# Optimization experiments

Measured on AMD Instinct MI355X. Metric: run time of the kernel, lower is better.

Reference implementation:

```python
import jax, jax.numpy as jnp
import numpy as np

N_POINTS = 300000
N_PAIRS = 100000  # rulebook pairs per kernel offset
K_OFFSETS = 27    # 3x3x3 kernel
C_IN, C_OUT = 32, 64
GROUPS = 8
EPS = 1e-5
NEG_SLOPE = 0.01


def setup_inputs() -> dict:
    key = jax.random.key(0)
    k1, k2, k3, k4 = jax.random.split(key, 4)
    feats = jax.random.normal(k1, (N_POINTS, C_IN), dtype=jnp.float32)
    weight = jax.random.normal(k2, (K_OFFSETS, C_IN, C_OUT), dtype=jnp.float32) * (1.0 / np.sqrt(C_IN * K_OFFSETS))
    gamma = jnp.ones((C_OUT,), dtype=jnp.float32)
    beta = jnp.zeros((C_OUT,), dtype=jnp.float32)
    in_idx = jax.random.randint(k3, (K_OFFSETS, N_PAIRS), 0, N_POINTS, dtype=jnp.int64)
    out_idx = jax.random.randint(k4, (K_OFFSETS, N_PAIRS), 0, N_POINTS, dtype=jnp.int64)
    return {"feats": feats, "weight": weight, "gamma": gamma, "beta": beta,
            "in_idx": in_idx, "out_idx": out_idx}


def reference(feats, weight, gamma, beta, in_idx, out_idx):
    # Sparse 3D conv via rulebook: gather -> per-offset matmul -> scatter-add
    gathered = feats[in_idx]                       # [K, P, C_in]
    y = jnp.einsum('kpi,kio->kpo', gathered, weight)  # [K, P, C_out]
    out = jnp.zeros((feats.shape[0], weight.shape[2]), feats.dtype)
    out = out.at[out_idx.reshape(-1)].add(y.reshape(-1, weight.shape[2]))
    # GroupNorm(8, C_out): stats over all points and channels within each group
    N, C = out.shape
    xg = out.reshape(N, GROUPS, C // GROUPS)
    mean = jnp.mean(xg, axis=(0, 2), keepdims=True)
    var = jnp.var(xg, axis=(0, 2), keepdims=True)
    xn = ((xg - mean) * jax.lax.rsqrt(var + EPS)).reshape(N, C)
    xn = xn * gamma + beta
    # LeakyReLU (default negative_slope = 0.01)
    return jnp.where(xn >= 0, xn, NEG_SLOPE * xn)
```

## Files before the change

kernel.cpp:

```cpp
#include <hip/hip_runtime.h>

#define NPTS   300000
#define NPAIRS 100000
#define KOFF   27
#define NTOT   (KOFF * NPAIRS)
#define CIN    32
#define COUT   64
#define NGROUP 8
#define EPSV   1e-5f
#define SLOPE  0.01f

#define PAIRS_PER_BLOCK 256
#define BLOCKS_PER_K ((NPAIRS + PAIRS_PER_BLOCK - 1) / PAIRS_PER_BLOCK)

#define NB1 293

#define OFS_STATS  0u
#define OFS_CURSOR 4096u
#define OFS_PART   (OFS_CURSOR + 1200128u)
#define OFS_PSLOT  (OFS_PART + 8192u)
#define OFS_SLOTS  (OFS_PSLOT + 10800128u)
#define OFS_FB16   (OFS_SLOTS + 345600000u)
#define WS_NEEDED  ((size_t)OFS_FB16 + 19200000u)

__device__ inline unsigned short f2b(float x) {
    unsigned u = __float_as_uint(x);
    u += 0x7FFFu + ((u >> 16) & 1u);
    return (unsigned short)(u >> 16);
}
__device__ inline float b2f_lo(unsigned d)  { return __uint_as_float(d << 16); }
__device__ inline float b2f_hi(unsigned d)  { return __uint_as_float(d & 0xFFFF0000u); }


__global__ __launch_bounds__(256) void to_bf16_kernel(const float2* __restrict__ src,
                                                      unsigned* __restrict__ dst, int n2) {
    int i = blockIdx.x * 256 + threadIdx.x;
    if (i < n2) {
        float2 v = src[i];
        dst[i] = (unsigned)f2b(v.x) | ((unsigned)f2b(v.y) << 16);
    }
}

__global__ __launch_bounds__(256) void zero_aux_kernel(int* __restrict__ cursor,
                                                       float* __restrict__ stats) {
    int i = blockIdx.x * 256 + threadIdx.x;
    if (i < NPTS) cursor[i] = 0;
    if (blockIdx.x == 0 && threadIdx.x < 16) stats[threadIdx.x] = 0.f;
}

__global__ __launch_bounds__(256) void hist_kernel(const int* __restrict__ oi,
                                                   int* __restrict__ cursor) {
    int i = blockIdx.x * 256 + threadIdx.x;
    if (i < NTOT) atomicAdd(cursor + oi[i], 1);
}

__global__ __launch_bounds__(256) void reduce_blocks_kernel(const int* __restrict__ cursor,
                                                            int* __restrict__ part) {
    __shared__ int sm[256];
    int tid = threadIdx.x, i0 = blockIdx.x * 1024 + tid * 4;
    int s = 0;
#pragma unroll
    for (int j = 0; j < 4; ++j) if (i0 + j < NPTS) s += cursor[i0 + j];
    sm[tid] = s; __syncthreads();
    for (int off = 128; off; off >>= 1) {
        if (tid < off) sm[tid] += sm[tid + off];
        __syncthreads();
    }
    if (tid == 0) part[blockIdx.x] = sm[0];
}

__global__ __launch_bounds__(512) void scan_partials_kernel(int* __restrict__ part) {
    __shared__ int sm[512];
    int tid = threadIdx.x;
    int v = (tid < NB1) ? part[tid] : 0;
    sm[tid] = v; __syncthreads();
    for (int off = 1; off < 512; off <<= 1) {
        int t = (tid >= off) ? sm[tid - off] : 0;
        __syncthreads();
        sm[tid] += t;
        __syncthreads();
    }
    if (tid < NB1) part[tid] = sm[tid] - v;
}

__global__ __launch_bounds__(256) void scan_apply_kernel(int* __restrict__ cursor,
                                                         const int* __restrict__ part) {
    __shared__ int sm[256];
    int tid = threadIdx.x, i0 = blockIdx.x * 1024 + tid * 4;
    int c0 = 0, c1 = 0, c2 = 0, c3 = 0;
    if (i0 + 0 < NPTS) c0 = cursor[i0 + 0];
    if (i0 + 1 < NPTS) c1 = cursor[i0 + 1];
    if (i0 + 2 < NPTS) c2 = cursor[i0 + 2];
    if (i0 + 3 < NPTS) c3 = cursor[i0 + 3];
    int s = c0 + c1 + c2 + c3;
    sm[tid] = s; __syncthreads();
    for (int off = 1; off < 256; off <<= 1) {
        int t = (tid >= off) ? sm[tid - off] : 0;
        __syncthreads();
        sm[tid] += t;
        __syncthreads();
    }
    int excl = sm[tid] - s + part[blockIdx.x];
    if (i0 + 0 < NPTS) cursor[i0 + 0] = excl;
    if (i0 + 1 < NPTS) cursor[i0 + 1] = excl + c0;
    if (i0 + 2 < NPTS) cursor[i0 + 2] = excl + c0 + c1;
    if (i0 + 3 < NPTS) cursor[i0 + 3] = excl + c0 + c1 + c2;
}

__global__ __launch_bounds__(256) void fill_kernel(const int* __restrict__ oi,
                                                   int* __restrict__ cursor,
                                                   int* __restrict__ pair_slot) {
    int i = blockIdx.x * 256 + threadIdx.x;
    if (i < NTOT) pair_slot[i] = atomicAdd(cursor + oi[i], 1);
}

__global__ __launch_bounds__(256) void convA_kernel(
    const unsigned* __restrict__ fb16, const float* __restrict__ weight,
    const int* __restrict__ in_idx, const int* __restrict__ pair_slot,
    unsigned short* __restrict__ slots16)
{
    const int lane = threadIdx.x & 63;
    const int wave = threadIdx.x >> 6;
    const int k     = blockIdx.x / BLOCKS_PER_K;
    const int pair0 = (blockIdx.x % BLOCKS_PER_K) * PAIRS_PER_BLOCK;

    float w[CIN];
    const float* wk = weight + k * (CIN * COUT) + lane;
#pragma unroll
    for (int i = 0; i < CIN; ++i) w[i] = wk[i * COUT];

    const int per_wave = PAIRS_PER_BLOCK / 4;
    int p    = pair0 + wave * per_wave;
    int pend = p + per_wave;
    if (pend > NPAIRS) pend = NPAIRS;

    const int* ii = in_idx    + k * NPAIRS;
    const int* ps = pair_slot + k * NPAIRS;

    for (; p < pend; ++p) {
        int rin  = __builtin_amdgcn_readfirstlane(ii[p]);
        int slot = __builtin_amdgcn_readfirstlane(ps[p]);
        const unsigned* fr = fb16 + rin * (CIN / 2);
        float acc = 0.f;
#pragma unroll
        for (int j = 0; j < CIN / 2; ++j) {
            unsigned d = fr[j];
            acc = fmaf(b2f_lo(d), w[2 * j],     acc);
            acc = fmaf(b2f_hi(d), w[2 * j + 1], acc);
        }
        slots16[(size_t)slot * COUT + lane] = f2b(acc);
    }
}

__global__ __launch_bounds__(256) void reduceB_kernel(const unsigned short* __restrict__ slots16,
                                                      const int* __restrict__ ends,
                                                      float* __restrict__ out)
{
    const int lane = threadIdx.x & 63;
    const int row  = blockIdx.x * 4 + (threadIdx.x >> 6);
    if (row >= NPTS) return;
    int e = ends[row];
    int s = (row == 0) ? 0 : ends[row - 1];
    float acc = 0.f;
    for (; s < e; ++s)
        acc += __uint_as_float(((unsigned)slots16[(size_t)s * COUT + lane]) << 16);
    out[(size_t)row * COUT + lane] = acc;
}

__global__ __launch_bounds__(256) void stats_kernel(const float* __restrict__ out,
                                                    float* __restrict__ stats) {
    const int c = threadIdx.x & 63;
    const int wave_in_grid = blockIdx.x * 4 + (threadIdx.x >> 6);
    const int nwaves = gridDim.x * 4;
    float s = 0.f, ss = 0.f;
    for (int r = wave_in_grid; r < NPTS; r += nwaves) {
        float v = out[(size_t)r * COUT + c];
        s += v; ss += v * v;
    }
#pragma unroll
    for (int m = 1; m < 8; m <<= 1) {
        s  += __shfl_xor(s,  m, 64);
        ss += __shfl_xor(ss, m, 64);
    }
    if ((c & 7) == 0) {
        int g = c >> 3;
        atomicAdd(stats + g,     s);
        atomicAdd(stats + 8 + g, ss);
    }
}

__global__ __launch_bounds__(256) void norm_kernel(float4* __restrict__ out4, int n4,
                                                   const float* __restrict__ stats,
                                                   const float* __restrict__ gamma,
                                                   const float* __restrict__ beta) {
    int i = blockIdx.x * blockDim.x + threadIdx.x;
    if (i >= n4) return;
    int c0 = (i & 15) * 4;
    int g  = c0 >> 3;
    const float cnt = (float)NPTS * (COUT / NGROUP);
    float mean = stats[g] / cnt;
    float var  = stats[8 + g] / cnt - mean * mean;
    float inv  = rsqrtf(var + EPSV);
    float4 v  = out4[i];
    float4 ga = *(const float4*)(gamma + c0);
    float4 be = *(const float4*)(beta  + c0);
    float x;
    x = (v.x - mean) * inv * ga.x + be.x; v.x = x >= 0.f ? x : SLOPE * x;
    x = (v.y - mean) * inv * ga.y + be.y; v.y = x >= 0.f ? x : SLOPE * x;
    x = (v.z - mean) * inv * ga.z + be.z; v.z = x >= 0.f ? x : SLOPE * x;
    x = (v.w - mean) * inv * ga.w + be.w; v.w = x >= 0.f ? x : SLOPE * x;
    out4[i] = v;
}

__global__ __launch_bounds__(256) void zero_out_kernel(float4* __restrict__ out4, int n4,
                                                       float* __restrict__ stats) {
    int i = blockIdx.x * blockDim.x + threadIdx.x;
    if (i < n4) out4[i] = make_float4(0.f, 0.f, 0.f, 0.f);
    if (blockIdx.x == 0 && threadIdx.x < 16) stats[threadIdx.x] = 0.f;
}

__global__ __launch_bounds__(256) void conv_atomic_kernel(
    const float* __restrict__ feats, const float* __restrict__ weight,
    const int* __restrict__ in_idx, const int* __restrict__ out_idx,
    float* __restrict__ out)
{
    const int lane = threadIdx.x & 63;
    const int wave = threadIdx.x >> 6;
    const int k     = blockIdx.x / BLOCKS_PER_K;
    const int pair0 = (blockIdx.x % BLOCKS_PER_K) * PAIRS_PER_BLOCK;
    float w[CIN];
    const float* wk = weight + k * (CIN * COUT) + lane;
#pragma unroll
    for (int i = 0; i < CIN; ++i) w[i] = wk[i * COUT];
    const int per_wave = PAIRS_PER_BLOCK / 4;
    int p = pair0 + wave * per_wave;
    int pend = p + per_wave;
    if (pend > NPAIRS) pend = NPAIRS;
    const int* ii = in_idx  + k * NPAIRS;
    const int* oi = out_idx + k * NPAIRS;
    for (; p < pend; ++p) {
        int rin  = __builtin_amdgcn_readfirstlane(ii[p]);
        int rout = __builtin_amdgcn_readfirstlane(oi[p]);
        const float* frow = feats + (size_t)rin * CIN;
        float acc = 0.f;
#pragma unroll
        for (int i = 0; i < CIN; ++i) acc = fmaf(frow[i], w[i], acc);
        atomicAdd(out + (size_t)rout * COUT + lane, acc);
    }
}

extern "C" void kernel_launch(void* const* d_in, const int* in_sizes, int n_in,
                              void* d_out, int out_size, void* d_ws, size_t ws_size,
                              hipStream_t stream) {
    const float* feats   = (const float*)d_in[0];
    const float* weight  = (const float*)d_in[1];
    const float* gamma   = (const float*)d_in[2];
    const float* beta    = (const float*)d_in[3];
    const int*   in_idx  = (const int*)d_in[4];
    const int*   out_idx = (const int*)d_in[5];
    float* out = (float*)d_out;

    char* ws = (char*)d_ws;
    float*          stats     = (float*)(ws + OFS_STATS);
    int*            cursor    = (int*)(ws + OFS_CURSOR);
    int*            part      = (int*)(ws + OFS_PART);
    int*            pair_slot = (int*)(ws + OFS_PSLOT);
    unsigned short* slots16   = (unsigned short*)(ws + OFS_SLOTS);
    unsigned*       fb16      = (unsigned*)(ws + OFS_FB16);

    int n4 = out_size / 4;
    int zb = (n4 + 255) / 256;

    if (ws_size >= WS_NEEDED) {
        int n2 = NPTS * CIN / 2;
        to_bf16_kernel<<<(n2 + 255) / 256, 256, 0, stream>>>((const float2*)feats, fb16, n2);
        zero_aux_kernel<<<(NPTS + 255) / 256, 256, 0, stream>>>(cursor, stats);
        hist_kernel<<<(NTOT + 255) / 256, 256, 0, stream>>>(out_idx, cursor);
        reduce_blocks_kernel<<<NB1, 256, 0, stream>>>(cursor, part);
        scan_partials_kernel<<<1, 512, 0, stream>>>(part);
        scan_apply_kernel<<<NB1, 256, 0, stream>>>(cursor, part);
        fill_kernel<<<(NTOT + 255) / 256, 256, 0, stream>>>(out_idx, cursor, pair_slot);
        convA_kernel<<<KOFF * BLOCKS_PER_K, 256, 0, stream>>>(fb16, weight, in_idx, pair_slot, slots16);
        reduceB_kernel<<<(NPTS + 3) / 4, 256, 0, stream>>>(slots16, cursor, out);
        stats_kernel<<<1024, 256, 0, stream>>>(out, stats);
        norm_kernel<<<zb, 256, 0, stream>>>((float4*)out, n4, stats, gamma, beta);
    } else {
        zero_out_kernel<<<zb, 256, 0, stream>>>((float4*)out, n4, stats);
        conv_atomic_kernel<<<KOFF * BLOCKS_PER_K, 256, 0, stream>>>(feats, weight, in_idx, out_idx, out);
        stats_kernel<<<1024, 256, 0, stream>>>(out, stats);
        norm_kernel<<<zb, 256, 0, stream>>>((float4*)out, n4, stats, gamma, beta);
    }
}
```

Baseline: 823.8 us.

## Replace slot-buffer scatter with CSR gather-conv fused with GroupNorm stats

The counting sort now stores packed (input index, offset) entries per output row instead of per-pair slot indices. A single CSR kernel walks each output row's entries, gathers fp16 features, and computes dot products against fp16 weights held in LDS using fdot2. It writes each output row once and accumulates the GroupNorm statistics in the same pass. This removes the large intermediate slots buffer and the separate reduce and stats kernels, at the cost of fp16 precision, a static per-wave row split that can load-balance poorly, and a sequential per-row loop.

Result: slower. 847.1 us (+2.8%).

```diff
diff --git a/kernel.cpp b/kernel.cpp
--- a/kernel.cpp
+++ b/kernel.cpp
@@ -12,33 +12,49 @@
 
 #define PAIRS_PER_BLOCK 256
 #define BLOCKS_PER_K ((NPAIRS + PAIRS_PER_BLOCK - 1) / PAIRS_PER_BLOCK)
-
 #define NB1 293
 
 #define OFS_STATS  0u
 #define OFS_CURSOR 4096u
-#define OFS_PART   (OFS_CURSOR + 1200128u)
-#define OFS_PSLOT  (OFS_PART + 8192u)
-#define OFS_SLOTS  (OFS_PSLOT + 10800128u)
-#define OFS_FB16   (OFS_SLOTS + 345600000u)
-#define WS_NEEDED  ((size_t)OFS_FB16 + 19200000u)
-
+#define OFS_PART   (OFS_CURSOR + 1204224u)
+#define OFS_ENT    (OFS_PART + 4096u)
+#define OFS_FH16   (OFS_ENT + 10850304u)
+#define WS_MAIN    ((size_t)OFS_FH16 + 19200000u)
+#define OFS_FB16_FB 4096u
+#define WS_BF16_FB ((size_t)OFS_FB16_FB + 19200000u)
+
+typedef _Float16 half2v __attribute__((ext_vector_type(2)));
+
+__device__ inline unsigned pack_h2(float a, float b) {
+    union { _Float16 h[2]; unsigned u; } x;
+    x.h[0] = (_Float16)a; x.h[1] = (_Float16)b;
+    return x.u;
+}
+__device__ inline half2v as_h2(unsigned u) {
+    union { unsigned u; half2v h; } x; x.u = u; return x.h;
+}
+__device__ inline float dot2_h(unsigned a, unsigned b, float c) {
+#if __has_builtin(__builtin_amdgcn_fdot2)
+    return __builtin_amdgcn_fdot2(as_h2(a), as_h2(b), c, false);
+#else
+    half2v ha = as_h2(a), hb = as_h2(b);
+    c = fmaf((float)ha.x, (float)hb.x, c);
+    return fmaf((float)ha.y, (float)hb.y, c);
+#endif
+}
 __device__ inline unsigned short f2b(float x) {
     unsigned u = __float_as_uint(x);
     u += 0x7FFFu + ((u >> 16) & 1u);
     return (unsigned short)(u >> 16);
 }
-__device__ inline float b2f_lo(unsigned d)  { return __uint_as_float(d << 16); }
-__device__ inline float b2f_hi(unsigned d)  { return __uint_as_float(d & 0xFFFF0000u); }
-
-
-__global__ __launch_bounds__(256) void to_bf16_kernel(const float2* __restrict__ src,
-                                                      unsigned* __restrict__ dst, int n2) {
-    int i = blockIdx.x * 256 + threadIdx.x;
-    if (i < n2) {
-        float2 v = src[i];
-        dst[i] = (unsigned)f2b(v.x) | ((unsigned)f2b(v.y) << 16);
-    }
+__device__ inline float b2f_lo(unsigned d) { return __uint_as_float(d << 16); }
+__device__ inline float b2f_hi(unsigned d) { return __uint_as_float(d & 0xFFFF0000u); }
+
+
+__global__ __launch_bounds__(256) void to_f16_kernel(const float2* __restrict__ src,
+                                                     unsigned* __restrict__ dst, int n2) {
+    int i = blockIdx.x * 256 + threadIdx.x;
+    if (i < n2) { float2 v = src[i]; dst[i] = pack_h2(v.x, v.y); }
 }
 
 __global__ __launch_bounds__(256) void zero_aux_kernel(int* __restrict__ cursor,
@@ -108,84 +124,84 @@
 }
 
 __global__ __launch_bounds__(256) void fill_kernel(const int* __restrict__ oi,
+                                                   const int* __restrict__ ii,
                                                    int* __restrict__ cursor,
-                                                   int* __restrict__ pair_slot) {
-    int i = blockIdx.x * 256 + threadIdx.x;
-    if (i < NTOT) pair_slot[i] = atomicAdd(cursor + oi[i], 1);
-}
-
-__global__ __launch_bounds__(256) void convA_kernel(
-    const unsigned* __restrict__ fb16, const float* __restrict__ weight,
-    const int* __restrict__ in_idx, const int* __restrict__ pair_slot,
-    unsigned short* __restrict__ slots16)
+                                                   unsigned* __restrict__ entries) {
+    int i = blockIdx.x * 256 + threadIdx.x;
+    if (i < NTOT) {
+        int k = i / NPAIRS;
+        int slot = atomicAdd(cursor + oi[i], 1);
+        entries[slot] = (unsigned)ii[i] | ((unsigned)k << 19);
+    }
+}
+
+__global__ __launch_bounds__(1024) void conv_csr_kernel(
+    const unsigned* __restrict__ fh16, const float* __restrict__ weight,
+    const unsigned* __restrict__ entries, const int* __restrict__ ends,
+    float* __restrict__ out, float* __restrict__ stats)
 {
-    const int lane = threadIdx.x & 63;
-    const int wave = threadIdx.x >> 6;
-    const int k     = blockIdx.x / BLOCKS_PER_K;
-    const int pair0 = (blockIdx.x % BLOCKS_PER_K) * PAIRS_PER_BLOCK;
-
-    float w[CIN];
-    const float* wk = weight + k * (CIN * COUT) + lane;
-#pragma unroll
-    for (int i = 0; i < CIN; ++i) w[i] = wk[i * COUT];
-
-    const int per_wave = PAIRS_PER_BLOCK / 4;
-    int p    = pair0 + wave * per_wave;
-    int pend = p + per_wave;
-    if (pend > NPAIRS) pend = NPAIRS;
-
-    const int* ii = in_idx    + k * NPAIRS;
-    const int* ps = pair_slot + k * NPAIRS;
-
-    for (; p < pend; ++p) {
-        int rin  = __builtin_amdgcn_readfirstlane(ii[p]);
-        int slot = __builtin_amdgcn_readfirstlane(ps[p]);
-        const unsigned* fr = fb16 + rin * (CIN / 2);
-        float acc = 0.f;
-#pragma unroll
-        for (int j = 0; j < CIN / 2; ++j) {
-            unsigned d = fr[j];
-            acc = fmaf(b2f_lo(d), w[2 * j],     acc);
-            acc = fmaf(b2f_hi(d), w[2 * j + 1], acc);
+    __shared__ unsigned lds_w[KOFF * 16 * 64];
+    const int tid = threadIdx.x;
+    for (int d = tid; d < KOFF * 1024; d += 1024) {
+        int k = d >> 10, rem = d & 1023, j = rem >> 6, c = rem & 63;
+        const float* wp = weight + k * (CIN * COUT) + (2 * j) * COUT + c;
+        lds_w[d] = pack_h2(wp[0], wp[COUT]);
+    }
+    __syncthreads();
+
+    const int lane = tid & 63;
+    const int gw   = blockIdx.x * 16 + (tid >> 6);
+    const int chunk = (NPTS + 4095) / 4096;
+    int rbeg = gw * chunk;
+    int rend = rbeg + chunk; if (rend > NPTS) rend = NPTS;
+
+    float ssum = 0.f, ssq = 0.f;
+
+    if (rbeg < NPTS) {
+        int s = (rbeg == 0) ? 0 : ends[rbeg - 1];
+        s = __builtin_amdgcn_readfirstlane(s);
+        for (int r = rbeg; r < rend; ++r) {
+            int e = __builtin_amdgcn_readfirstlane(ends[r]);
+            float acc = 0.f;
+            if (s < e) {
+                unsigned ent = __builtin_amdgcn_readfirstlane(entries[s]);
+                unsigned f[16];
+                {
+                    const unsigned* fr = fh16 + (size_t)(ent & 0x7FFFFu) * 16;
+#pragma unroll
+                    for (int j = 0; j < 16; ++j) f[j] = fr[j];
+                }
+                for (int t = s; t < e; ++t) {
+                    unsigned nent = (t + 1 < e)
+                        ? __builtin_amdgcn_readfirstlane(entries[t + 1]) : ent;
+                    unsigned g[16];
+                    const unsigned* nr = fh16 + (size_t)(nent & 0x7FFFFu) * 16;
+#pragma unroll
+                    for (int j = 0; j < 16; ++j) g[j] = nr[j];
+                    int kk = ent >> 19;
+                    const unsigned* wl = lds_w + (kk << 10) + lane;
+#pragma unroll
+                    for (int j = 0; j < 16; ++j)
+                        acc = dot2_h(f[j], wl[j << 6], acc);
+#pragma unroll
+                    for (int j = 0; j < 16; ++j) f[j] = g[j];
+                    ent = nent;
+                }
+            }
+            out[(size_t)r * COUT + lane] = acc;
+            ssum += acc; ssq += acc * acc;
+            s = e;
         }
-        slots16[(size_t)slot * COUT + lane] = f2b(acc);
-    }
-}
-
-__global__ __launch_bounds__(256) void reduceB_kernel(const unsigned short* __restrict__ slots16,
-                                                      const int* __restrict__ ends,
-                                                      float* __restrict__ out)
-{
-    const int lane = threadIdx.x & 63;
-    const int row  = blockIdx.x * 4 + (threadIdx.x >> 6);
-    if (row >= NPTS) return;
-    int e = ends[row];
-    int s = (row == 0) ? 0 : ends[row - 1];
-    float acc = 0.f;
-    for (; s < e; ++s)
-        acc += __uint_as_float(((unsigned)slots16[(size_t)s * COUT + lane]) << 16);
-    out[(size_t)row * COUT + lane] = acc;
-}
-
-__global__ __launch_bounds__(256) void stats_kernel(const float* __restrict__ out,
-                                                    float* __restrict__ stats) {
-    const int c = threadIdx.x & 63;
-    const int wave_in_grid = blockIdx.x * 4 + (threadIdx.x >> 6);
-    const int nwaves = gridDim.x * 4;
-    float s = 0.f, ss = 0.f;
-    for (int r = wave_in_grid; r < NPTS; r += nwaves) {
-        float v = out[(size_t)r * COUT + c];
-        s += v; ss += v * v;
     }
 #pragma unroll
     for (int m = 1; m < 8; m <<= 1) {
-        s  += __shfl_xor(s,  m, 64);
-        ss += __shfl_xor(ss, m, 64);
-    }
-    if ((c & 7) == 0) {
-        int g = c >> 3;
-        atomicAdd(stats + g,     s);
-        atomicAdd(stats + 8 + g, ss);
+        ssum += __shfl_xor(ssum, m, 64);
+        ssq  += __shfl_xor(ssq,  m, 64);
+    }
+    if ((lane & 7) == 0) {
+        int g = lane >> 3;
+        atomicAdd(stats + g,     ssum);
+        atomicAdd(stats + 8 + g, ssq);
     }
 }
 
@@ -212,14 +228,56 @@
     out4[i] = v;
 }
 
-__global__ __launch_bounds__(256) void zero_out_kernel(float4* __restrict__ out4, int n4,
-                                                       float* __restrict__ stats) {
+__global__ __launch_bounds__(256) void zero_kernel(float4* __restrict__ out4, int n4,
+                                                   float* __restrict__ stats) {
     int i = blockIdx.x * blockDim.x + threadIdx.x;
     if (i < n4) out4[i] = make_float4(0.f, 0.f, 0.f, 0.f);
     if (blockIdx.x == 0 && threadIdx.x < 16) stats[threadIdx.x] = 0.f;
 }
 
-__global__ __launch_bounds__(256) void conv_atomic_kernel(
+__global__ __launch_bounds__(256) void to_bf16_kernel(const float2* __restrict__ src,
+                                                      unsigned* __restrict__ dst, int n2) {
+    int i = blockIdx.x * 256 + threadIdx.x;
+    if (i < n2) {
+        float2 v = src[i];
+        dst[i] = (unsigned)f2b(v.x) | ((unsigned)f2b(v.y) << 16);
+    }
+}
+
+__global__ __launch_bounds__(256) void conv_bf16_kernel(
+    const unsigned* __restrict__ fb16, const float* __restrict__ weight,
+    const int* __restrict__ in_idx, const int* __restrict__ out_idx,
+    float* __restrict__ out)
+{
+    const int lane = threadIdx.x & 63;
+    const int wave = threadIdx.x >> 6;
+    const int k     = blockIdx.x / BLOCKS_PER_K;
+    const int pair0 = (blockIdx.x % BLOCKS_PER_K) * PAIRS_PER_BLOCK;
+    float w[CIN];
+    const float* wk = weight + k * (CIN * COUT) + lane;
+#pragma unroll
+    for (int i = 0; i < CIN; ++i) w[i] = wk[i * COUT];
+    const int per_wave = PAIRS_PER_BLOCK / 4;
+    int p = pair0 + wave * per_wave;
+    int pend = p + per_wave; if (pend > NPAIRS) pend = NPAIRS;
+    const int* ii = in_idx  + k * NPAIRS;
+    const int* oi = out_idx + k * NPAIRS;
+    for (; p < pend; ++p) {
+        int rin  = __builtin_amdgcn_readfirstlane(ii[p]);
+        int rout = __builtin_amdgcn_readfirstlane(oi[p]);
+        const unsigned* fr = fb16 + (size_t)rin * (CIN / 2);
+        float acc = 0.f;
+#pragma unroll
+        for (int j = 0; j < CIN / 2; ++j) {
+            unsigned d = fr[j];
+            acc = fmaf(b2f_lo(d), w[2 * j],     acc);
+            acc = fmaf(b2f_hi(d), w[2 * j + 1], acc);
+        }
+        atomicAdd(out + (size_t)rout * COUT + lane, acc);
+    }
+}
+
+__global__ __launch_bounds__(256) void conv_f32_kernel(
     const float* __restrict__ feats, const float* __restrict__ weight,
     const int* __restrict__ in_idx, const int* __restrict__ out_idx,
     float* __restrict__ out)
@@ -234,8 +292,7 @@
     for (int i = 0; i < CIN; ++i) w[i] = wk[i * COUT];
     const int per_wave = PAIRS_PER_BLOCK / 4;
     int p = pair0 + wave * per_wave;
-    int pend = p + per_wave;
-    if (pend > NPAIRS) pend = NPAIRS;
+    int pend = p + per_wave; if (pend > NPAIRS) pend = NPAIRS;
     const int* ii = in_idx  + k * NPAIRS;
     const int* oi = out_idx + k * NPAIRS;
     for (; p < pend; ++p) {
@@ -246,6 +303,28 @@
 #pragma unroll
         for (int i = 0; i < CIN; ++i) acc = fmaf(frow[i], w[i], acc);
         atomicAdd(out + (size_t)rout * COUT + lane, acc);
+    }
+}
+
+__global__ __launch_bounds__(256) void stats_kernel(const float* __restrict__ out,
+                                                    float* __restrict__ stats) {
+    const int c = threadIdx.x & 63;
+    const int wave_in_grid = blockIdx.x * 4 + (threadIdx.x >> 6);
+    const int nwaves = gridDim.x * 4;
+    float s = 0.f, ss = 0.f;
+    for (int r = wave_in_grid; r < NPTS; r += nwaves) {
+        float v = out[(size_t)r * COUT + c];
+        s += v; ss += v * v;
+    }
+#pragma unroll
+    for (int m = 1; m < 8; m <<= 1) {
+        s  += __shfl_xor(s,  m, 64);
+        ss += __shfl_xor(ss, m, 64);
+    }
+    if ((c & 7) == 0) {
+        int g = c >> 3;
+        atomicAdd(stats + g,     s);
+        atomicAdd(stats + 8 + g, ss);
     }
 }
 
@@ -259,35 +338,41 @@
     const int*   in_idx  = (const int*)d_in[4];
     const int*   out_idx = (const int*)d_in[5];
     float* out = (float*)d_out;
-
-    char* ws = (char*)d_ws;
-    float*          stats     = (float*)(ws + OFS_STATS);
-    int*            cursor    = (int*)(ws + OFS_CURSOR);
-    int*            part      = (int*)(ws + OFS_PART);
-    int*            pair_slot = (int*)(ws + OFS_PSLOT);
-    unsigned short* slots16   = (unsigned short*)(ws + OFS_SLOTS);
-    unsigned*       fb16      = (unsigned*)(ws + OFS_FB16);
+    char*  ws  = (char*)d_ws;
 
     int n4 = out_size / 4;
     int zb = (n4 + 255) / 256;
-
-    if (ws_size >= WS_NEEDED) {
-        int n2 = NPTS * CIN / 2;
-        to_bf16_kernel<<<(n2 + 255) / 256, 256, 0, stream>>>((const float2*)feats, fb16, n2);
-        zero_aux_kernel<<<(NPTS + 255) / 256, 256, 0, stream>>>(cursor, stats);
+    int n2 = NPTS * CIN / 2;
+
+    if (ws_size >= WS_MAIN) {
+        float*    stats   = (float*)(ws + OFS_STATS);
+        int*      cursor  = (int*)(ws + OFS_CURSOR);
+        int*      part    = (int*)(ws + OFS_PART);
+        unsigned* entries = (unsigned*)(ws + OFS_ENT);
+        unsigned* fh16    = (unsigned*)(ws + OFS_FH16);
+
+        to_f16_kernel<<<(n2 + 255) / 256, 256, 0, stream>>>((const float2*)feats, fh16, n2);
+        zero_aux_kernel<<<(NPTS + 255) / 256, 256, 0, stream>>>(cursor, (float*)(ws + OFS_STATS));
         hist_kernel<<<(NTOT + 255) / 256, 256, 0, stream>>>(out_idx, cursor);
         reduce_blocks_kernel<<<NB1, 256, 0, stream>>>(cursor, part);
         scan_partials_kernel<<<1, 512, 0, stream>>>(part);
         scan_apply_kernel<<<NB1, 256, 0, stream>>>(cursor, part);
-        fill_kernel<<<(NTOT + 255) / 256, 256, 0, stream>>>(out_idx, cursor, pair_slot);
-        convA_kernel<<<KOFF * BLOCKS_PER_K, 256, 0, stream>>>(fb16, weight, in_idx, pair_slot, slots16);
-        reduceB_kernel<<<(NPTS + 3) / 4, 256, 0, stream>>>(slots16, cursor, out);
-        stats_kernel<<<1024, 256, 0, stream>>>(out, stats);
+        fill_kernel<<<(NTOT + 255) / 256, 256, 0, stream>>>(out_idx, in_idx, cursor, entries);
+        conv_csr_kernel<<<256, 1024, 0, stream>>>(fh16, weight, entries, cursor, out, stats);
+        norm_kernel<<<zb, 256, 0, stream>>>((float4*)out, n4, stats, gamma, beta);
+    } else if (ws_size >= WS_BF16_FB) {
+        float*    stats = (float*)(ws + OFS_STATS);
+        unsigned* fb16  = (unsigned*)(ws + OFS_FB16_FB);
+        zero_kernel<<<zb, 256, 0, stream>>>((float4*)out, n4, stats);
+        to_bf16_kernel<<<(n2 + 255) / 256, 256, 0, stream>>>((const float2*)feats, fb16, n2);
+        conv_bf16_kernel<<<KOFF * BLOCKS_PER_K, 256, 0, stream>>>(fb16, weight, in_idx, out_idx, out);
+        stats_kernel<<<2048, 256, 0, stream>>>(out, stats);
         norm_kernel<<<zb, 256, 0, stream>>>((float4*)out, n4, stats, gamma, beta);
     } else {
-        zero_out_kernel<<<zb, 256, 0, stream>>>((float4*)out, n4, stats);
-        conv_atomic_kernel<<<KOFF * BLOCKS_PER_K, 256, 0, stream>>>(feats, weight, in_idx, out_idx, out);
-        stats_kernel<<<1024, 256, 0, stream>>>(out, stats);
+        float* stats = (float*)(ws + OFS_STATS);
+        zero_kernel<<<zb, 256, 0, stream>>>((float4*)out, n4, stats);
+        conv_f32_kernel<<<KOFF * BLOCKS_PER_K, 256, 0, stream>>>(feats, weight, in_idx, out_idx, out);
+        stats_kernel<<<2048, 256, 0, stream>>>(out, stats);
         norm_kernel<<<zb, 256, 0, stream>>>((float4*)out, n4, stats, gamma, beta);
     }
 }
```
